# Optimization experiments

Hardware: AMD Instinct MI355X
Metric: run time of the kernel (lower is better)

The kernel has to match this reference:

```python
import jax, jax.numpy as jnp
import numpy as np

N = 100000
E = 1600000
H = 128


def setup_inputs() -> dict:
    key = jax.random.key(0)
    k1, k2, k3 = jax.random.split(key, 3)
    x = jax.random.normal(k1, (N, H), dtype=jnp.float32)
    edge_index = jax.random.randint(k2, (2, E), 0, N, dtype=jnp.int64)
    W = jax.random.normal(k3, (H, H), dtype=jnp.float32) / np.sqrt(H)
    b = jnp.zeros((H,), dtype=jnp.float32)
    gamma = jnp.ones((H,), dtype=jnp.float32)
    beta = jnp.zeros((H,), dtype=jnp.float32)
    return {"x": x, "edge_index": edge_index, "W": W, "b": b, "gamma": gamma, "beta": beta}


def reference(x, edge_index, W, b, gamma, beta):
    n = x.shape[0]
    # Linear transform first (standard GCNConv order)
    h = x @ W  # [N, H]
    # Add self loops
    loop = jnp.arange(n, dtype=edge_index.dtype)
    src = jnp.concatenate([edge_index[0], loop])
    dst = jnp.concatenate([edge_index[1], loop])
    # Symmetric degree normalization: deg computed over destination index
    ones = jnp.ones(src.shape[0], dtype=x.dtype)
    deg = jax.ops.segment_sum(ones, dst, num_segments=n)  # [N]
    dinv = jnp.where(deg > 0, jax.lax.rsqrt(deg), jnp.zeros_like(deg))
    norm = dinv[src] * dinv[dst]  # [E+N]
    # Gather, scale, scatter-add
    msgs = h[src] * norm[:, None]  # [E+N, H]
    out = jax.ops.segment_sum(msgs, dst, num_segments=n) + b  # [N, H]
    # GELU (exact erf form, matching torch F.gelu default)
    out = jax.nn.gelu(out, approximate=False)
    # LayerNorm over feature dim
    mu = jnp.mean(out, axis=-1, keepdims=True)
    var = jnp.mean(jnp.square(out - mu), axis=-1, keepdims=True)
    out = (out - mu) * jax.lax.rsqrt(var + 1e-5) * gamma + beta
    # Dropout is identity in eval mode
    return out
```

## Files before the change

### kernel.cpp

```cpp
#include <hip/hip_runtime.h>
#include <math.h>

#define H 128
#define PART_EDGES 8192
#define SORT_LDS 4096

typedef __bf16 bf16x8 __attribute__((ext_vector_type(8)));
typedef float f32x4 __attribute__((ext_vector_type(4)));
typedef _Float16 h2 __attribute__((ext_vector_type(2)));
typedef __attribute__((address_space(3))) unsigned lds_u32;
typedef __attribute__((address_space(1))) const unsigned glob_u32;

static __device__ __forceinline__ unsigned short f2bf(float f) {
    unsigned u = __float_as_uint(f);
    unsigned r = 0x7fffu + ((u >> 16) & 1u);
    return (unsigned short)((u + r) >> 16);
}
static __device__ __forceinline__ unsigned packh2(float a, float b) {
    h2 h = { (_Float16)a, (_Float16)b };
    return __builtin_bit_cast(unsigned, h);
}
static __device__ __forceinline__ h2 u2h(unsigned w) {
    return __builtin_bit_cast(h2, w);
}
static __device__ __forceinline__ float gelu_f(float v) {
    float z  = v * 0.70710678118654752f;
    float az = fabsf(z);
    float t  = __frcp_rn(1.0f + 0.3275911f * az);
    float p  = t * (0.254829592f + t * (-0.284496736f + t * (1.421413741f +
               t * (-1.453152027f + t * 1.061405429f))));
    float e  = p * __expf(-az * az);
    float erf = 1.0f - e;
    erf = (z < 0.0f) ? -erf : erf;
    return 0.5f * v * (1.0f + erf);
}

__global__ __launch_bounds__(512) void k_bhist(const int* __restrict__ dst,
                                               int* __restrict__ bcnt_pad,
                                               int E, int NBUK) {
    __shared__ int lh[1024];
    int t = threadIdx.x;
    for (int i = t; i < 1024; i += 512) lh[i] = 0;
    __syncthreads();
    int e0 = blockIdx.x * PART_EDGES;
    int e1 = min(e0 + PART_EDGES, E);
    for (int e = e0 + t; e < e1; e += 512) atomicAdd(&lh[dst[e] >> 7], 1);
    __syncthreads();
    for (int i = t; i < NBUK; i += 512) {
        int h = lh[i];
        if (h) atomicAdd(&bcnt_pad[i * 16], h);
    }
}

__global__ __launch_bounds__(1024) void k_bscan(const int* __restrict__ bcnt_pad,
                                                int* __restrict__ boff,
                                                int* __restrict__ bcur,
                                                int* __restrict__ rowp,
                                                int NBUK, int N, int E) {
    __shared__ int tmp[1024];
    __shared__ int carry;
    int t = threadIdx.x;
    if (t == 0) carry = 0;
    __syncthreads();
    for (int base = 0; base < NBUK; base += 1024) {
        int i = base + t;
        int v = (i < NBUK) ? bcnt_pad[i * 16] : 0;
        tmp[t] = v;
        __syncthreads();
#pragma unroll
        for (int off = 1; off < 1024; off <<= 1) {
            int a = (t >= off) ? tmp[t - off] : 0;
            __syncthreads();
            tmp[t] += a;
            __syncthreads();
        }
        int excl = carry + tmp[t] - v;
        if (i < NBUK) { boff[i] = excl; bcur[i] = excl; }
        __syncthreads();
        if (t == 1023) carry += tmp[1023];
        __syncthreads();
    }
    if (t == 0) { boff[NBUK] = carry; rowp[N] = E; }
}

__global__ void k_wt(const float* __restrict__ W, unsigned short* __restrict__ Wsz) {
    int t = blockIdx.x * 256 + threadIdx.x;
    int j = t >> 7, k = t & 127;
    unsigned byte = (unsigned)(j * 256 + 2 * k) ^ (((unsigned)j & 7u) << 4);
    *(unsigned short*)((char*)Wsz + byte) = f2bf(W[(size_t)k * H + j]);
}

__global__ void k_xb(const float* __restrict__ x, const float* __restrict__ dinv,
                     unsigned* __restrict__ xb2, int N) {
    int t = blockIdx.x * 256 + threadIdx.x;
    if (t >= N * 32) return;
    int n = t >> 5;
    float s = dinv[n];
    float4 v = ((const float4*)x)[t];
    uint2 o;
    o.x = packh2(v.x * s, v.y * s);
    o.y = packh2(v.z * s, v.w * s);
    ((uint2*)xb2)[t] = o;
}

__global__ __launch_bounds__(512) void k_part(const int* __restrict__ ei,
                                              int* __restrict__ bcur,
                                              unsigned* __restrict__ pair, int E) {
    __shared__ int hist[1024];
    __shared__ int base[1024];
    int t = threadIdx.x;
    for (int i = t; i < 1024; i += 512) hist[i] = 0;
    __syncthreads();
    int e0 = blockIdx.x * PART_EDGES;
    int e1 = min(e0 + PART_EDGES, E);
    for (int e = e0 + t; e < e1; e += 512) {
        int d = ei[E + e];
        atomicAdd(&hist[d >> 7], 1);
    }
    __syncthreads();
    for (int i = t; i < 1024; i += 512) {
        int h = hist[i];
        base[i] = h ? atomicAdd(&bcur[i], h) : 0;
        hist[i] = 0;
    }
    __syncthreads();
    for (int e = e0 + t; e < e1; e += 512) {
        int s = ei[e];
        int d = ei[E + e];
        int b = d >> 7;
        int r = atomicAdd(&hist[b], 1);
        pair[base[b] + r] = (unsigned)s | ((unsigned)(d & 127) << 17);
    }
}

__global__ __launch_bounds__(256) void k_sort(const unsigned* __restrict__ pair,
                                              const int* __restrict__ boff,
                                              int* __restrict__ rowp,
                                              int* __restrict__ ssrc,
                                              float* __restrict__ dinv, int N) {
    __shared__ int hist[128];
    __shared__ int lofs[128];
    __shared__ int cur[128];
    __shared__ int sl[SORT_LDS];
    int b = blockIdx.x;
    int t = threadIdx.x;
    int lo = boff[b], hi = boff[b + 1];
    int cntE = hi - lo;
    if (t < 128) hist[t] = 0;
    __syncthreads();
    for (int i = t; i < cntE; i += 256) {
        unsigned w = pair[lo + i];
        atomicAdd(&hist[w >> 17], 1);
    }
    __syncthreads();
    int n0 = b << 7;
    if (t < 128 && n0 + t < N) dinv[n0 + t] = rsqrtf((float)(hist[t] + 1));
    if (t == 0) {
        int run = 0;
        for (int d = 0; d < 128; ++d) { lofs[d] = run; cur[d] = run; run += hist[d]; }
    }
    __syncthreads();
    if (t < 128 && n0 + t < N) rowp[n0 + t] = lo + lofs[t];
    for (int i = t; i < cntE; i += 256) {
        unsigned w = pair[lo + i];
        int d = w >> 17;
        int s = (int)(w & 0x1FFFF);
        int pos = atomicAdd(&cur[d], 1);
        if (pos < SORT_LDS) sl[pos] = s;
        else ssrc[lo + pos] = s;
    }
    __syncthreads();
    int lim = min(cntE, SORT_LDS);
    for (int i = t; i < lim; i += 256) ssrc[lo + i] = sl[i];
}

__global__ __launch_bounds__(256) void k_agg(const unsigned* __restrict__ xb2,
                                             const int* __restrict__ rowp,
                                             const int* __restrict__ ssrc,
                                             const float* __restrict__ dinv,
                                             unsigned* __restrict__ aggb2, int N) {
    int n = blockIdx.x * 4 + (threadIdx.x >> 6);
    if (n >= N) return;
    int lane = threadIdx.x & 63;
    int grp  = lane >> 4;
    int sub  = lane & 15;

    int lo = __builtin_amdgcn_readfirstlane(rowp[n]);
    int hi = __builtin_amdgcn_readfirstlane(rowp[n + 1]);
    float dn = dinv[n];

    h2 acc[4];
#pragma unroll
    for (int i = 0; i < 4; ++i) acc[i] = (h2){ (_Float16)0, (_Float16)0 };

    if (grp == 0) {
        uint4 sw = ((const uint4*)(xb2 + (size_t)n * 64))[sub];
        acc[0] = u2h(sw.x); acc[1] = u2h(sw.y);
        acc[2] = u2h(sw.z); acc[3] = u2h(sw.w);
    }

    for (int base = lo; base < hi; base += 64) {
        int take = hi - base; if (take > 64) take = 64;
        int sv = ssrc[base + (lane < take ? lane : take - 1)];

        int nFull = take >> 3;
        for (int it = 0; it < nFull; ++it) {
            int p1 = (it << 3) + grp;
            int p2 = p1 + 4;
            int s1 = __builtin_amdgcn_ds_bpermute(p1 << 2, sv);
            int s2 = __builtin_amdgcn_ds_bpermute(p2 << 2, sv);
            uint4 w1 = ((const uint4*)(xb2 + (size_t)s1 * 64))[sub];
            uint4 w2 = ((const uint4*)(xb2 + (size_t)s2 * 64))[sub];
            acc[0] += u2h(w1.x); acc[1] += u2h(w1.y);
            acc[2] += u2h(w1.z); acc[3] += u2h(w1.w);
            acc[0] += u2h(w2.x); acc[1] += u2h(w2.y);
            acc[2] += u2h(w2.z); acc[3] += u2h(w2.w);
        }
        if (take & 7) {
            int p1 = (nFull << 3) + grp;
            int p2 = p1 + 4;
            int q1 = (p1 < take) ? p1 : take - 1;
            int q2 = (p2 < take) ? p2 : take - 1;
            int s1 = __builtin_amdgcn_ds_bpermute(q1 << 2, sv);
            int s2 = __builtin_amdgcn_ds_bpermute(q2 << 2, sv);
            if (p1 < take) {
                uint4 w1 = ((const uint4*)(xb2 + (size_t)s1 * 64))[sub];
                acc[0] += u2h(w1.x); acc[1] += u2h(w1.y);
                acc[2] += u2h(w1.z); acc[3] += u2h(w1.w);
            }
            if (p2 < take) {
                uint4 w2 = ((const uint4*)(xb2 + (size_t)s2 * 64))[sub];
                acc[0] += u2h(w2.x); acc[1] += u2h(w2.y);
                acc[2] += u2h(w2.z); acc[3] += u2h(w2.w);
            }
        }
    }

#pragma unroll
    for (int i = 0; i < 4; ++i) {
        unsigned au = __builtin_bit_cast(unsigned, acc[i]);
        acc[i] += u2h((unsigned)__shfl_xor((int)au, 16, 64));
        au = __builtin_bit_cast(unsigned, acc[i]);
        acc[i] += u2h((unsigned)__shfl_xor((int)au, 32, 64));
    }

    if (grp == 0) {
        uint4 o;
        o.x = (unsigned)f2bf((float)acc[0][0] * dn) | ((unsigned)f2bf((float)acc[0][1] * dn) << 16);
        o.y = (unsigned)f2bf((float)acc[1][0] * dn) | ((unsigned)f2bf((float)acc[1][1] * dn) << 16);
        o.z = (unsigned)f2bf((float)acc[2][0] * dn) | ((unsigned)f2bf((float)acc[2][1] * dn) << 16);
        o.w = (unsigned)f2bf((float)acc[3][0] * dn) | ((unsigned)f2bf((float)acc[3][1] * dn) << 16);
        ((uint4*)(aggb2 + (size_t)n * 64))[sub] = o;
    }
}

__global__ __launch_bounds__(512) void k_gemm_ln(const unsigned short* __restrict__ aggb,
                                                 const unsigned short* __restrict__ Wsz,
                                                 const float* __restrict__ bias,
                                                 const float* __restrict__ gamma,
                                                 const float* __restrict__ beta,
                                                 float* __restrict__ outp,
                                                 int N) {
    __shared__ unsigned short Ws[H * H];

    const int wv   = threadIdx.x >> 6;
    const int lane = threadIdx.x & 63;
    const int g    = lane >> 4;
    const int c    = lane & 15;
    const int r0   = blockIdx.x * 128 + wv * 16;

    int ar = r0 + c; if (ar >= N) ar = N - 1;
    bf16x8 af[4];
#pragma unroll
    for (int ks = 0; ks < 4; ++ks)
        af[ks] = *(const bf16x8*)(aggb + (size_t)ar * H + ks * 32 + g * 8);

#pragma unroll
    for (int it = 0; it < 4; ++it) {
        int off = it * 8192 + wv * 1024;
        __builtin_amdgcn_global_load_lds(
            (glob_u32*)((const char*)Wsz + off + lane * 16),
            (lds_u32*)((char*)Ws + off), 16, 0, 0);
    }
    __syncthreads();

    if (r0 < N) {
        float bc[8], gc[8], bec[8];
#pragma unroll
        for (int ct = 0; ct < 8; ++ct) {
            int col = ct * 16 + c;
            bc[ct]  = bias[col];
            gc[ct]  = gamma[col];
            bec[ct] = beta[col];
        }

        f32x4 acc[8];
#pragma unroll
        for (int ct = 0; ct < 8; ++ct) acc[ct] = (f32x4){0.f, 0.f, 0.f, 0.f};

#pragma unroll
        for (int ks = 0; ks < 4; ++ks) {
#pragma unroll
            for (int ct = 0; ct < 8; ++ct) {
                int j = ct * 16 + c;
                int byte = (j * 256 + ks * 64 + g * 16) ^ ((j & 7) << 4);
                bf16x8 bf = *(const bf16x8*)((const char*)Ws + byte);
                acc[ct] = __builtin_amdgcn_mfma_f32_16x16x32_bf16(af[ks], bf, acc[ct], 0, 0, 0);
            }
        }

#pragma unroll
        for (int q = 0; q < 4; ++q) {
            int row = r0 + g * 4 + q;
            float v[8];
            float s = 0.f, sq = 0.f;
#pragma unroll
            for (int ct = 0; ct < 8; ++ct) {
                float t = gelu_f(acc[ct][q] + bc[ct]);
                v[ct] = t;
                s += t;
                sq += t * t;
            }
#pragma unroll
            for (int off = 8; off > 0; off >>= 1) {
                s  += __shfl_xor(s,  off, 64);
                sq += __shfl_xor(sq, off, 64);
            }
            float mu  = s * (1.0f / H);
            float var = sq * (1.0f / H) - mu * mu;
            float rs  = rsqrtf(var + 1e-5f);
            if (row < N) {
                float* op = outp + (size_t)row * H;
#pragma unroll
                for (int ct = 0; ct < 8; ++ct) {
                    op[ct * 16 + c] = (v[ct] - mu) * rs * gc[ct] + bec[ct];
                }
            }
        }
    }
}

extern "C" void kernel_launch(void* const* d_in, const int* in_sizes, int n_in,
                              void* d_out, int out_size, void* d_ws, size_t ws_size,
                              hipStream_t stream) {
    const float* x     = (const float*)d_in[0];
    const int*   ei    = (const int*)d_in[1];
    const float* W     = (const float*)d_in[2];
    const float* b     = (const float*)d_in[3];
    const float* gamma = (const float*)d_in[4];
    const float* beta  = (const float*)d_in[5];
    float* out = (float*)d_out;

    const int N = in_sizes[0] / H;
    const int E = in_sizes[1] / 2;
    const int NBUK = (N + 127) / 128;

    char* w = (char*)d_ws;
    auto alloc = [&](size_t bytes) {
        char* p = w;
        w += (bytes + 255) & ~(size_t)255;
        return p;
    };
    float* dinv     = (float*)alloc((size_t)N * 4);
    int*   bcnt_pad = (int*)alloc((size_t)NBUK * 16 * 4);
    int*   boff     = (int*)alloc((size_t)(NBUK + 1) * 4);
    int*   bcur     = (int*)alloc((size_t)NBUK * 4);
    int*   rowp     = (int*)alloc((size_t)(N + 1) * 4);
    int*   ssrc     = (int*)alloc((size_t)E * 4);
    unsigned short* Wsz = (unsigned short*)alloc((size_t)H * H * 2);
    unsigned* aggb2 = (unsigned*)alloc((size_t)N * 64 * 4);

    unsigned* xb2  = (unsigned*)d_out;
    unsigned* pair = (unsigned*)d_out + (size_t)N * 64;

    k_wt   <<<(H * H) / 256, 256, 0, stream>>>(W, Wsz);

    hipMemsetAsync(bcnt_pad, 0, (size_t)NBUK * 16 * 4, stream);
    k_bhist<<<(E + PART_EDGES - 1) / PART_EDGES, 512, 0, stream>>>(ei + E, bcnt_pad, E, NBUK);
    k_bscan<<<1, 1024, 0, stream>>>(bcnt_pad, boff, bcur, rowp, NBUK, N, E);
    k_part <<<(E + PART_EDGES - 1) / PART_EDGES, 512, 0, stream>>>(ei, bcur, pair, E);
    k_sort <<<NBUK, 256, 0, stream>>>(pair, boff, rowp, ssrc, dinv, N);
    k_xb   <<<(N * 32 + 255) / 256, 256, 0, stream>>>(x, dinv, xb2, N);

    k_agg  <<<(N + 3) / 4, 256, 0, stream>>>(xb2, rowp, ssrc, dinv, aggb2, N);

    k_gemm_ln<<<(N + 127) / 128, 512, 0, stream>>>((const unsigned short*)aggb2, Wsz,
                                                   b, gamma, beta, out, N);
}
```

Measured before the change: 152.4 us.

## Split feature matrix into 8 column slices for cache-local gather aggregation

Reorganizes the fp16 scaled features into eight 16-column slices stored contiguously per slice, and launches eight times as many aggregation blocks, each gathering a single slice. A slice is 32 bytes per node (about 3.2MB for all nodes), so the working set of each concurrent pass can stay in L2 instead of thrashing across the full 25MB table. The GEMM input load is remapped to read the sliced aggregation layout. In exchange, the CSR row pointers and edge indices are re-read eight times, the per-edge gathers become 32-byte accesses, and more shuffle reduction steps are needed.

```diff
diff --git a/kernel.cpp b/kernel.cpp
--- a/kernel.cpp
+++ b/kernel.cpp
@@ -91,16 +91,20 @@
 }
 
 __global__ void k_xb(const float* __restrict__ x, const float* __restrict__ dinv,
-                     unsigned* __restrict__ xb2, int N) {
+                     unsigned* __restrict__ xbs, int N) {
     int t = blockIdx.x * 256 + threadIdx.x;
     if (t >= N * 32) return;
-    int n = t >> 5;
+    int slice = t / (N * 4);
+    int r     = t - slice * (N * 4);
+    int n     = r >> 2;
+    int w2    = r & 3;
     float s = dinv[n];
-    float4 v = ((const float4*)x)[t];
+    const float* xp = x + (size_t)n * H + slice * 16 + w2 * 4;
+    float4 v = *(const float4*)xp;
     uint2 o;
     o.x = packh2(v.x * s, v.y * s);
     o.y = packh2(v.z * s, v.w * s);
-    ((uint2*)xb2)[t] = o;
+    *(uint2*)(xbs + (size_t)slice * N * 8 + (size_t)n * 8 + w2 * 2) = o;
 }
 
 __global__ __launch_bounds__(512) void k_part(const int* __restrict__ ei,
@@ -174,87 +178,68 @@
     for (int i = t; i < lim; i += 256) ssrc[lo + i] = sl[i];
 }
 
-__global__ __launch_bounds__(256) void k_agg(const unsigned* __restrict__ xb2,
+__global__ __launch_bounds__(256) void k_agg(const unsigned* __restrict__ xbs,
                                              const int* __restrict__ rowp,
                                              const int* __restrict__ ssrc,
                                              const float* __restrict__ dinv,
-                                             unsigned* __restrict__ aggb2, int N) {
-    int n = blockIdx.x * 4 + (threadIdx.x >> 6);
+                                             unsigned* __restrict__ aggs, int N) {
+    int slice = blockIdx.x & 7;
+    int n = (blockIdx.x >> 3) * 4 + (threadIdx.x >> 6);
     if (n >= N) return;
     int lane = threadIdx.x & 63;
-    int grp  = lane >> 4;
-    int sub  = lane & 15;
+    int e = lane >> 3;
+    int p = lane & 7;
+
+    const unsigned* sb = xbs + (size_t)slice * N * 8;
 
     int lo = __builtin_amdgcn_readfirstlane(rowp[n]);
     int hi = __builtin_amdgcn_readfirstlane(rowp[n + 1]);
-    float dn = dinv[n];
-
-    h2 acc[4];
-#pragma unroll
-    for (int i = 0; i < 4; ++i) acc[i] = (h2){ (_Float16)0, (_Float16)0 };
-
-    if (grp == 0) {
-        uint4 sw = ((const uint4*)(xb2 + (size_t)n * 64))[sub];
-        acc[0] = u2h(sw.x); acc[1] = u2h(sw.y);
-        acc[2] = u2h(sw.z); acc[3] = u2h(sw.w);
-    }
+
+    h2 acc1 = (h2){ (_Float16)0, (_Float16)0 };
+    h2 acc2 = (h2){ (_Float16)0, (_Float16)0 };
+
+    if (lane < 8) acc1 = u2h(sb[(size_t)n * 8 + lane]);
 
     for (int base = lo; base < hi; base += 64) {
         int take = hi - base; if (take > 64) take = 64;
         int sv = ssrc[base + (lane < take ? lane : take - 1)];
 
-        int nFull = take >> 3;
-        for (int it = 0; it < nFull; ++it) {
-            int p1 = (it << 3) + grp;
-            int p2 = p1 + 4;
-            int s1 = __builtin_amdgcn_ds_bpermute(p1 << 2, sv);
-            int s2 = __builtin_amdgcn_ds_bpermute(p2 << 2, sv);
-            uint4 w1 = ((const uint4*)(xb2 + (size_t)s1 * 64))[sub];
-            uint4 w2 = ((const uint4*)(xb2 + (size_t)s2 * 64))[sub];
-            acc[0] += u2h(w1.x); acc[1] += u2h(w1.y);
-            acc[2] += u2h(w1.z); acc[3] += u2h(w1.w);
-            acc[0] += u2h(w2.x); acc[1] += u2h(w2.y);
-            acc[2] += u2h(w2.z); acc[3] += u2h(w2.w);
-        }
-        if (take & 7) {
-            int p1 = (nFull << 3) + grp;
-            int p2 = p1 + 4;
+        int nF2 = take >> 4;
+        for (int it = 0; it < nF2; ++it) {
+            int s1 = __builtin_amdgcn_ds_bpermute((it * 16 + e) << 2, sv);
+            int s2 = __builtin_amdgcn_ds_bpermute((it * 16 + 8 + e) << 2, sv);
+            acc1 += u2h(sb[(size_t)s1 * 8 + p]);
+            acc2 += u2h(sb[(size_t)s2 * 8 + p]);
+        }
+        int rem = take - (nF2 << 4);
+        if (rem) {
+            int p1 = (nF2 << 4) + e;
+            int p2 = p1 + 8;
             int q1 = (p1 < take) ? p1 : take - 1;
             int q2 = (p2 < take) ? p2 : take - 1;
             int s1 = __builtin_amdgcn_ds_bpermute(q1 << 2, sv);
             int s2 = __builtin_amdgcn_ds_bpermute(q2 << 2, sv);
-            if (p1 < take) {
-                uint4 w1 = ((const uint4*)(xb2 + (size_t)s1 * 64))[sub];
-                acc[0] += u2h(w1.x); acc[1] += u2h(w1.y);
-                acc[2] += u2h(w1.z); acc[3] += u2h(w1.w);
-            }
-            if (p2 < take) {
-                uint4 w2 = ((const uint4*)(xb2 + (size_t)s2 * 64))[sub];
-                acc[0] += u2h(w2.x); acc[1] += u2h(w2.y);
-                acc[2] += u2h(w2.z); acc[3] += u2h(w2.w);
-            }
-        }
-    }
-
-#pragma unroll
-    for (int i = 0; i < 4; ++i) {
-        unsigned au = __builtin_bit_cast(unsigned, acc[i]);
-        acc[i] += u2h((unsigned)__shfl_xor((int)au, 16, 64));
-        au = __builtin_bit_cast(unsigned, acc[i]);
-        acc[i] += u2h((unsigned)__shfl_xor((int)au, 32, 64));
-    }
-
-    if (grp == 0) {
-        uint4 o;
-        o.x = (unsigned)f2bf((float)acc[0][0] * dn) | ((unsigned)f2bf((float)acc[0][1] * dn) << 16);
-        o.y = (unsigned)f2bf((float)acc[1][0] * dn) | ((unsigned)f2bf((float)acc[1][1] * dn) << 16);
-        o.z = (unsigned)f2bf((float)acc[2][0] * dn) | ((unsigned)f2bf((float)acc[2][1] * dn) << 16);
-        o.w = (unsigned)f2bf((float)acc[3][0] * dn) | ((unsigned)f2bf((float)acc[3][1] * dn) << 16);
-        ((uint4*)(aggb2 + (size_t)n * 64))[sub] = o;
-    }
-}
-
-__global__ __launch_bounds__(512) void k_gemm_ln(const unsigned short* __restrict__ aggb,
+            if (p1 < take) acc1 += u2h(sb[(size_t)s1 * 8 + p]);
+            if (p2 < take) acc2 += u2h(sb[(size_t)s2 * 8 + p]);
+        }
+    }
+
+    h2 acc = acc1 + acc2;
+#pragma unroll
+    for (int off = 8; off <= 32; off <<= 1) {
+        unsigned au = __builtin_bit_cast(unsigned, acc);
+        acc += u2h((unsigned)__shfl_xor((int)au, off, 64));
+    }
+
+    if (lane < 8) {
+        float dn = dinv[n];
+        unsigned o = (unsigned)f2bf((float)acc[0] * dn) |
+                     ((unsigned)f2bf((float)acc[1] * dn) << 16);
+        aggs[(size_t)slice * N * 8 + (size_t)n * 8 + lane] = o;
+    }
+}
+
+__global__ __launch_bounds__(512) void k_gemm_ln(const unsigned* __restrict__ aggs,
                                                  const unsigned short* __restrict__ Wsz,
                                                  const float* __restrict__ bias,
                                                  const float* __restrict__ gamma,
@@ -272,8 +257,10 @@
     int ar = r0 + c; if (ar >= N) ar = N - 1;
     bf16x8 af[4];
 #pragma unroll
-    for (int ks = 0; ks < 4; ++ks)
-        af[ks] = *(const bf16x8*)(aggb + (size_t)ar * H + ks * 32 + g * 8);
+    for (int ks = 0; ks < 4; ++ks) {
+        int slice = 2 * ks + (g >> 1);
+        af[ks] = *(const bf16x8*)(aggs + (size_t)slice * N * 8 + (size_t)ar * 8 + (g & 1) * 4);
+    }
 
 #pragma unroll
     for (int it = 0; it < 4; ++it) {
@@ -368,9 +355,9 @@
     int*   rowp     = (int*)alloc((size_t)(N + 1) * 4);
     int*   ssrc     = (int*)alloc((size_t)E * 4);
     unsigned short* Wsz = (unsigned short*)alloc((size_t)H * H * 2);
-    unsigned* aggb2 = (unsigned*)alloc((size_t)N * 64 * 4);
-
-    unsigned* xb2  = (unsigned*)d_out;
+    unsigned* aggs  = (unsigned*)alloc((size_t)N * 64 * 4);
+
+    unsigned* xbs  = (unsigned*)d_out;
     unsigned* pair = (unsigned*)d_out + (size_t)N * 64;
 
     k_wt   <<<(H * H) / 256, 256, 0, stream>>>(W, Wsz);
@@ -380,10 +367,10 @@
     k_bscan<<<1, 1024, 0, stream>>>(bcnt_pad, boff, bcur, rowp, NBUK, N, E);
     k_part <<<(E + PART_EDGES - 1) / PART_EDGES, 512, 0, stream>>>(ei, bcur, pair, E);
     k_sort <<<NBUK, 256, 0, stream>>>(pair, boff, rowp, ssrc, dinv, N);
-    k_xb   <<<(N * 32 + 255) / 256, 256, 0, stream>>>(x, dinv, xb2, N);
-
-    k_agg  <<<(N + 3) / 4, 256, 0, stream>>>(xb2, rowp, ssrc, dinv, aggb2, N);
-
-    k_gemm_ln<<<(N + 127) / 128, 512, 0, stream>>>((const unsigned short*)aggb2, Wsz,
+    k_xb   <<<(N * 32 + 255) / 256, 256, 0, stream>>>(x, dinv, xbs, N);
+
+    k_agg  <<<((N + 3) / 4) * 8, 256, 0, stream>>>(xbs, rowp, ssrc, dinv, aggs, N);
+
+    k_gemm_ln<<<(N + 127) / 128, 512, 0, stream>>>(aggs, Wsz,
                                                    b, gamma, beta, out, N);
 }
```

Measured after the change: 293.4 us. +92.6%, slower.
